# Kernel tuning notes

Measured on AMD Instinct MI355X. Metric: run time of the kernel, lower is better.

Reference implementation:

```python
import jax, jax.numpy as jnp
import numpy as np

N = 50000
E = 800000
BN_EPS = 1e-5


def setup_inputs() -> dict:
    key = jax.random.key(0)
    ks = jax.random.split(key, 8)
    x = jax.random.normal(ks[0], (N, 64), dtype=jnp.float32)
    edge_index = jax.random.randint(ks[1], (2, E), 0, N, dtype=jnp.int64)
    edge_attr = jax.random.uniform(ks[2], (E,), dtype=jnp.float32)
    # GraphConv layer 1: lin_rel (with bias) + lin_root (no bias), 64 -> 128
    W1_rel = jax.random.normal(ks[3], (64, 128), dtype=jnp.float32) / np.sqrt(64)
    b1 = jnp.zeros((128,), dtype=jnp.float32)
    W1_root = jax.random.normal(ks[4], (64, 128), dtype=jnp.float32) / np.sqrt(64)
    # BatchNorm1d(128) affine params
    gamma = jnp.ones((128,), dtype=jnp.float32)
    beta = jnp.zeros((128,), dtype=jnp.float32)
    # GraphConv layer 2: 128 -> 32
    W2_rel = jax.random.normal(ks[5], (128, 32), dtype=jnp.float32) / np.sqrt(128)
    b2 = jnp.zeros((32,), dtype=jnp.float32)
    W2_root = jax.random.normal(ks[6], (128, 32), dtype=jnp.float32) / np.sqrt(128)
    return {"x": x, "edge_attr": edge_attr, "W1_rel": W1_rel, "b1": b1,
            "W1_root": W1_root, "gamma": gamma, "beta": beta,
            "W2_rel": W2_rel, "b2": b2, "W2_root": W2_root,
            "edge_index": edge_index}


def graph_conv(x, edge_index, edge_weight, W_rel, b_rel, W_root):
    # PyG GraphConv (aggr='add'): out = lin_rel(scatter_add(w_e * x[src] -> dst)) + lin_root(x)
    src, dst = edge_index[0], edge_index[1]
    msg = x[src] * edge_weight[:, None]              # [E, F] gather + scale
    agg = jax.ops.segment_sum(msg, dst, num_segments=x.shape[0])  # [N, F]
    return agg @ W_rel + b_rel + x @ W_root


def batch_norm_train(h, gamma, beta):
    mean = jnp.mean(h, axis=0)
    var = jnp.var(h, axis=0)  # biased, as torch uses for normalization
    return (h - mean) * jax.lax.rsqrt(var + BN_EPS) * gamma + beta


def reference(x, edge_attr, W1_rel, b1, W1_root, gamma, beta, W2_rel, b2, W2_root, edge_index):
    h = graph_conv(x, edge_index, edge_attr, W1_rel, b1, W1_root)
    h = batch_norm_train(h, gamma, beta)
    h = jnp.tanh(h)
    out = graph_conv(h, edge_index, edge_attr, W2_rel, b2, W2_root)
    return out
```

## Files before the change

kernel.cpp:

```cpp
#include <hip/hip_runtime.h>
#include <hip/hip_bf16.h>


#define NB 256
#define CAPB 4096
#define LCAP 16
#define CHUNK 2048
#define CAP 32
#define MAXROWS 196
#define OVF_CAP 131072

typedef __bf16 bf16x8 __attribute__((ext_vector_type(8)));
typedef float f32x4 __attribute__((ext_vector_type(4)));

__device__ __forceinline__ void atomAdd(float* p, float v) { unsafeAtomicAdd(p, v); }

__device__ __forceinline__ unsigned packrec(unsigned src, float w) {
    __bf16 bw = (__bf16)w;
    unsigned short us = *(unsigned short*)&bw;
    return (src << 16) | (unsigned)us;
}

__global__ __launch_bounds__(256) void init_k(
    const float* __restrict__ W1rel, const float* __restrict__ W1root,
    const float* __restrict__ W2rel, const float* __restrict__ W2root,
    __bf16* __restrict__ W1t, __bf16* __restrict__ W2t,
    int* __restrict__ gcnt, int* __restrict__ ovfcnt,
    float* __restrict__ bnsum, float* __restrict__ bnsq) {
    if (blockIdx.x == 0) {
        int t = threadIdx.x;
        if (t < NB) gcnt[t] = 0;
        if (t == 0) *ovfcnt = 0;
        if (t < 128) { bnsum[t] = 0.f; bnsq[t] = 0.f; }
    }
    int idx = blockIdx.x * 256 + threadIdx.x;
    if (idx < 128 * 128) {
        int n = idx >> 7, k = idx & 127;
        float v = (k < 64) ? W1rel[k * 128 + n] : W1root[(k - 64) * 128 + n];
        W1t[n * 128 + k] = (__bf16)v;
    } else if (idx < 128 * 128 + 64 * 128) {
        int j = idx - 128 * 128;
        int n = j >> 7, k = j & 127;
        float v = (n < 32) ? W2rel[k * 32 + n] : W2root[k * 32 + (n - 32)];
        W2t[n * 128 + k] = (__bf16)v;
    }
}

__global__ __launch_bounds__(256) void partx_k(
    const float* __restrict__ x, __bf16* __restrict__ xb, int xcB,
    const float* __restrict__ ea, const void* __restrict__ ei,
    int* __restrict__ gcnt, uint2* __restrict__ part,
    int* __restrict__ ovfcnt, int4* __restrict__ ovf, int E, int N) {
    __shared__ int s_flag;
    __shared__ int hist[NB];
    __shared__ int gb[NB];
    __shared__ uint2 stage[NB * LCAP];

    if ((int)blockIdx.x < xcB) {
        int j = blockIdx.x * 256 + threadIdx.x;
        if (j < N * 8) {
            const float4* xs = (const float4*)(x + (size_t)j * 8);
            float4 a = xs[0], b = xs[1];
            bf16x8 v;
            v[0] = (__bf16)a.x; v[1] = (__bf16)a.y; v[2] = (__bf16)a.z; v[3] = (__bf16)a.w;
            v[4] = (__bf16)b.x; v[5] = (__bf16)b.y; v[6] = (__bf16)b.z; v[7] = (__bf16)b.w;
            *(bf16x8*)(xb + (size_t)j * 8) = v;
        }
        return;
    }
    const int pb = blockIdx.x - xcB;

    if (threadIdx.x < 64) {
        const long long* p = (const long long*)ei;
        long long v = p[threadIdx.x & 15];
        int ok = (v >= 0 && v < (long long)N);
        unsigned long long m = __ballot(ok);
        if (threadIdx.x == 0) s_flag = (~m == 0ull) ? 1 : 0;
    }
    for (int i = threadIdx.x; i < NB; i += 256) hist[i] = 0;
    __syncthreads();
    const bool is64 = (s_flag != 0);

    const int base = pb * CHUNK + threadIdx.x * 8;
    int n = E - base; n = n < 0 ? 0 : (n > 8 ? 8 : n);

    int srcs[8], dsts[8]; float wv[8];
    if (n > 0) {
        if (is64) {
            const long long* p = (const long long*)ei;
            if (n == 8 && ((E & 1) == 0)) {
#pragma unroll
                for (int k = 0; k < 4; k++) {
                    int4 a = *(const int4*)(p + base + 2 * k);
                    srcs[2 * k] = a.x; srcs[2 * k + 1] = a.z;
                }
#pragma unroll
                for (int k = 0; k < 4; k++) {
                    int4 b = *(const int4*)(p + E + base + 2 * k);
                    dsts[2 * k] = b.x; dsts[2 * k + 1] = b.z;
                }
            } else {
                for (int k = 0; k < n; k++) { srcs[k] = (int)p[base + k]; dsts[k] = (int)p[E + base + k]; }
            }
        } else {
            const int* p = (const int*)ei;
            if (n == 8 && ((E & 3) == 0)) {
                int4 a0 = *(const int4*)(p + base);
                int4 a1 = *(const int4*)(p + base + 4);
                srcs[0] = a0.x; srcs[1] = a0.y; srcs[2] = a0.z; srcs[3] = a0.w;
                srcs[4] = a1.x; srcs[5] = a1.y; srcs[6] = a1.z; srcs[7] = a1.w;
                int4 b0 = *(const int4*)(p + E + base);
                int4 b1 = *(const int4*)(p + E + base + 4);
                dsts[0] = b0.x; dsts[1] = b0.y; dsts[2] = b0.z; dsts[3] = b0.w;
                dsts[4] = b1.x; dsts[5] = b1.y; dsts[6] = b1.z; dsts[7] = b1.w;
            } else {
                for (int k = 0; k < n; k++) { srcs[k] = p[base + k]; dsts[k] = p[E + base + k]; }
            }
        }
        if (n == 8) {
            float4 w0 = *(const float4*)(ea + base);
            float4 w1 = *(const float4*)(ea + base + 4);
            wv[0] = w0.x; wv[1] = w0.y; wv[2] = w0.z; wv[3] = w0.w;
            wv[4] = w1.x; wv[5] = w1.y; wv[6] = w1.z; wv[7] = w1.w;
        } else {
            for (int k = 0; k < n; k++) wv[k] = ea[base + k];
        }

        int bk[8], pos[8], loc[8];
#pragma unroll
        for (int k = 0; k < 8; k++) {
            if (k < n) {
                unsigned b = ((unsigned)dsts[k] << 8) / (unsigned)N;
                int r0 = (int)((b * (unsigned)N + 255u) >> 8);
                bk[k] = (int)b;
                loc[k] = dsts[k] - r0;
                pos[k] = atomicAdd(&hist[b], 1);
            }
        }
#pragma unroll
        for (int k = 0; k < 8; k++) {
            if (k < n) {
                unsigned packed = ((unsigned)loc[k] << 24) | (unsigned)srcs[k];
                if (pos[k] < LCAP) {
                    stage[bk[k] * LCAP + pos[k]] = make_uint2(packed, __float_as_uint(wv[k]));
                } else {
                    int g = atomicAdd(&gcnt[bk[k]], 1);
                    if (g < CAPB) {
                        part[(size_t)bk[k] * CAPB + g] = make_uint2(packed, __float_as_uint(wv[k]));
                    } else {
                        int o = atomicAdd(ovfcnt, 1);
                        if (o < OVF_CAP) ovf[o] = make_int4(srcs[k], dsts[k], (int)__float_as_uint(wv[k]), 0);
                    }
                }
            }
        }
    }
    __syncthreads();
    if (threadIdx.x < NB) {
        int h = hist[threadIdx.x]; if (h > LCAP) h = LCAP;
        hist[threadIdx.x] = h;
        gb[threadIdx.x] = h ? atomicAdd(&gcnt[threadIdx.x], h) : 0;
    }
    __syncthreads();
    const int wvi = threadIdx.x >> 6;
    const int sub = (threadIdx.x >> 4) & 3;
    const int f = threadIdx.x & 15;
    for (int round = 0; round < 16; ++round) {
        int b = wvi * 64 + round * 4 + sub;
        int h = hist[b];
        if (f < h) {
            int g = gb[b] + f;
            uint2 r = stage[b * LCAP + f];
            if (g < CAPB) {
                part[(size_t)b * CAPB + g] = r;
            } else {
                int r0 = (b * N + 255) >> 8;
                int dst = r0 + (int)(r.x >> 24);
                int o = atomicAdd(ovfcnt, 1);
                if (o < OVF_CAP) ovf[o] = make_int4((int)(r.x & 0xFFFFFFu), dst, (int)r.y, 0);
            }
        }
    }
}

__global__ __launch_bounds__(256) void binscat_k(
    const int* __restrict__ gcnt, const uint2* __restrict__ part,
    unsigned* __restrict__ bins, int* __restrict__ cnt,
    int* __restrict__ ovfcnt, int4* __restrict__ ovf, int N) {
    __shared__ unsigned stage[MAXROWS * CAP];
    __shared__ int lcnt[MAXROWS];
    const int b = blockIdx.x;
    const int r0 = (b * N + 255) >> 8;
    int r1 = ((b + 1) * N + 255) >> 8; if (r1 > N) r1 = N;
    const int rows = r1 - r0;
    for (int i = threadIdx.x; i < rows; i += 256) lcnt[i] = 0;
    __syncthreads();

    int m = gcnt[b]; if (m > CAPB) m = CAPB;
    const uint2* pb = part + (size_t)b * CAPB;
    for (int i = threadIdx.x; i < m; i += 256) {
        uint2 r = pb[i];
        int d = r.x >> 24;
        unsigned src = r.x & 0xFFFFFFu;
        float w = __uint_as_float(r.y);
        int pos = atomicAdd(&lcnt[d], 1);
        if (pos < CAP) {
            stage[d * CAP + pos] = packrec(src, w);
        } else {
            int o = atomicAdd(ovfcnt, 1);
            if (o < OVF_CAP) ovf[o] = make_int4((int)src, r0 + d, (int)r.y, 0);
        }
    }
    __syncthreads();
    uint4* dst = (uint4*)(bins + (size_t)r0 * CAP);
    const uint4* srcp = (const uint4*)stage;
    for (int i = threadIdx.x; i < rows * (CAP / 4); i += 256) dst[i] = srcp[i];
    for (int i = threadIdx.x; i < rows; i += 256) cnt[r0 + i] = lcnt[i];
}

__global__ __launch_bounds__(256) void spmm1_k(
    const __bf16* __restrict__ xb, const int* __restrict__ cntg,
    const unsigned* __restrict__ bins, const int* __restrict__ ovfcnt,
    const int4* __restrict__ ovf, __bf16* __restrict__ aggb, int N) {
    const int lane = threadIdx.x & 63;
    const int sub = lane >> 5;
    const int fp = lane & 31;
    const int row = (blockIdx.x * 256 + threadIdx.x) >> 6;
    if (row >= N) return;
    int cf = cntg[row];
    int cnt = cf > CAP ? CAP : cf;
    unsigned eg = 0u;
    if (lane < cnt) eg = bins[(size_t)row * CAP + lane];
    float ax = 0.f, ay = 0.f;
    for (int j = 0; j < cnt; j += 8) {
        int ss[4]; float ww[4]; unsigned uv[4];
#pragma unroll
        for (int k = 0; k < 4; k++) {
            int idx = j + 2 * k + sub;
            bool ok = idx < cnt;
            unsigned r = (unsigned)__shfl((int)eg, idx);
            ss[k] = ok ? (int)(r >> 16) : 0;
            ww[k] = ok ? __uint_as_float((r & 0xFFFFu) << 16) : 0.f;
        }
#pragma unroll
        for (int k = 0; k < 4; k++)
            uv[k] = *(const unsigned*)((const char*)xb + (size_t)ss[k] * 128 + fp * 4);
#pragma unroll
        for (int k = 0; k < 4; k++) {
            ax = fmaf(ww[k], __uint_as_float((uv[k] & 0xFFFFu) << 16), ax);
            ay = fmaf(ww[k], __uint_as_float(uv[k] & 0xFFFF0000u), ay);
        }
    }
    if (cf > CAP && sub == 0) {
        int nv = *ovfcnt; if (nv > OVF_CAP) nv = OVF_CAP;
        for (int i = 0; i < nv; i++) {
            int4 t = ovf[i];
            if (t.y == row) {
                float w = __uint_as_float((unsigned)t.z);
                unsigned u = *(const unsigned*)((const char*)xb + (size_t)t.x * 128 + fp * 4);
                ax = fmaf(w, __uint_as_float((u & 0xFFFFu) << 16), ax);
                ay = fmaf(w, __uint_as_float(u & 0xFFFF0000u), ay);
            }
        }
    }
    ax += __shfl_xor(ax, 32);
    ay += __shfl_xor(ay, 32);
    if (sub == 0) {
        __bf16 b0 = (__bf16)ax, b1 = (__bf16)ay;
        unsigned pack = (unsigned)*(unsigned short*)&b0 |
                        ((unsigned)*(unsigned short*)&b1 << 16);
        *(unsigned*)((char*)aggb + (size_t)row * 128 + fp * 4) = pack;
    }
}

__global__ __launch_bounds__(256) void gemm1_k(
    const __bf16* __restrict__ aggb, const __bf16* __restrict__ xb,
    const __bf16* __restrict__ W1t, const float* __restrict__ b1,
    __bf16* __restrict__ hb, float* __restrict__ bnsum, float* __restrict__ bnsq,
    int N) {
    __shared__ char Wl[128 * 256];
    __shared__ float redS[4][128];
    __shared__ float redQ[4][128];
    const int t = threadIdx.x;
    for (int i = t; i < 2048; i += 256) {
        int byte = i * 16;
        int row = byte >> 8;
        int sw = byte ^ ((row & 7) << 4);
        *(uint4*)(Wl + sw) = *(const uint4*)((const char*)W1t + byte);
    }

    const int lane = t & 63;
    const int w = t >> 6;
    const int rrow = lane & 15;
    const int q = lane >> 4;
    const int rowbase = blockIdx.x * 128 + w * 32;
    const int ar0 = rowbase + rrow;
    const int ar1 = rowbase + 16 + rrow;
    const int ar0c = (ar0 < N) ? ar0 : (N - 1);
    const int ar1c = (ar1 < N) ? ar1 : (N - 1);

    f32x4 acc0[8], acc1[8];
#pragma unroll
    for (int cb = 0; cb < 8; cb++) {
        acc0[cb][0] = 0.f; acc0[cb][1] = 0.f; acc0[cb][2] = 0.f; acc0[cb][3] = 0.f;
        acc1[cb][0] = 0.f; acc1[cb][1] = 0.f; acc1[cb][2] = 0.f; acc1[cb][3] = 0.f;
    }
    __syncthreads();

#pragma unroll
    for (int ks = 0; ks < 4; ks++) {
        const int koff = (ks & 1) * 32 + q * 8;
        const __bf16* base = (ks < 2) ? aggb : xb;
        bf16x8 a0 = *(const bf16x8*)(base + (size_t)ar0c * 64 + koff);
        bf16x8 a1 = *(const bf16x8*)(base + (size_t)ar1c * 64 + koff);
#pragma unroll
        for (int cb = 0; cb < 8; cb++) {
            int byte = (cb * 16 + rrow) * 256 + ks * 64 + q * 16;
            byte ^= ((rrow & 7) << 4);
            bf16x8 b = *(const bf16x8*)(Wl + byte);
            acc0[cb] = __builtin_amdgcn_mfma_f32_16x16x32_bf16(a0, b, acc0[cb], 0, 0, 0);
            acc1[cb] = __builtin_amdgcn_mfma_f32_16x16x32_bf16(a1, b, acc1[cb], 0, 0, 0);
        }
    }

    float s[8], qs[8];
#pragma unroll
    for (int cb = 0; cb < 8; cb++) {
        const int col = cb * 16 + rrow;
        const float bc = b1[col];
        float ls = 0.f, lq = 0.f;
#pragma unroll
        for (int r = 0; r < 4; r++) {
            int rr0 = rowbase + 4 * q + r;
            if (rr0 < N) {
                float v = acc0[cb][r] + bc;
                hb[(size_t)rr0 * 128 + col] = (__bf16)v;
                ls += v; lq += v * v;
            }
            int rr1 = rowbase + 16 + 4 * q + r;
            if (rr1 < N) {
                float v = acc1[cb][r] + bc;
                hb[(size_t)rr1 * 128 + col] = (__bf16)v;
                ls += v; lq += v * v;
            }
        }
        s[cb] = ls; qs[cb] = lq;
    }
#pragma unroll
    for (int cb = 0; cb < 8; cb++) {
        s[cb] += __shfl_xor(s[cb], 16);  s[cb] += __shfl_xor(s[cb], 32);
        qs[cb] += __shfl_xor(qs[cb], 16); qs[cb] += __shfl_xor(qs[cb], 32);
    }
    if (q == 0) {
#pragma unroll
        for (int cb = 0; cb < 8; cb++) {
            redS[w][cb * 16 + rrow] = s[cb];
            redQ[w][cb * 16 + rrow] = qs[cb];
        }
    }
    __syncthreads();
    if (t < 128) {
        atomAdd(&bnsum[t], redS[0][t] + redS[1][t] + redS[2][t] + redS[3][t]);
    } else {
        int c = t - 128;
        atomAdd(&bnsq[c], redQ[0][c] + redQ[1][c] + redQ[2][c] + redQ[3][c]);
    }
}

__global__ __launch_bounds__(256) void gemm2_k(
    const __bf16* __restrict__ hb, const float* __restrict__ bnsum,
    const float* __restrict__ bnsq, const float* __restrict__ gamma,
    const float* __restrict__ beta, const __bf16* __restrict__ W2t,
    const float* __restrict__ b2, __bf16* __restrict__ y2b,
    float* __restrict__ out, int N) {
    __shared__ char Wl[64 * 256];
    __shared__ float scs[128], shs[128];
    const int t = threadIdx.x;
    for (int i = t; i < 1024; i += 256) {
        int byte = i * 16;
        int row = byte >> 8;
        int sw = byte ^ ((row & 7) << 4);
        *(uint4*)(Wl + sw) = *(const uint4*)((const char*)W2t + byte);
    }
    if (t < 128) {
        float inv = 1.0f / (float)N;
        float mean = bnsum[t] * inv;
        float var = bnsq[t] * inv - mean * mean;
        if (var < 0.f) var = 0.f;
        float sc = gamma[t] * rsqrtf(var + 1e-5f);
        scs[t] = sc;
        shs[t] = beta[t] - mean * sc;
    }

    const int lane = t & 63;
    const int w = t >> 6;
    const int rrow = lane & 15;
    const int q = lane >> 4;
    const int rowbase = blockIdx.x * 128 + w * 32;
    const int ar0 = rowbase + rrow;
    const int ar1 = rowbase + 16 + rrow;
    const int ar0c = (ar0 < N) ? ar0 : (N - 1);
    const int ar1c = (ar1 < N) ? ar1 : (N - 1);

    f32x4 acc0[4], acc1[4];
#pragma unroll
    for (int cb = 0; cb < 4; cb++) {
        acc0[cb][0] = 0.f; acc0[cb][1] = 0.f; acc0[cb][2] = 0.f; acc0[cb][3] = 0.f;
        acc1[cb][0] = 0.f; acc1[cb][1] = 0.f; acc1[cb][2] = 0.f; acc1[cb][3] = 0.f;
    }
    __syncthreads();

#pragma unroll
    for (int ks = 0; ks < 4; ks++) {
        const int k0 = ks * 32 + q * 8;
        bf16x8 hv0 = *(const bf16x8*)(hb + (size_t)ar0c * 128 + k0);
        bf16x8 hv1 = *(const bf16x8*)(hb + (size_t)ar1c * 128 + k0);
        bf16x8 a0, a1;
#pragma unroll
        for (int i = 0; i < 8; i++) {
            float sc = scs[k0 + i], sh = shs[k0 + i];
            a0[i] = (__bf16)tanhf(fmaf((float)hv0[i], sc, sh));
            a1[i] = (__bf16)tanhf(fmaf((float)hv1[i], sc, sh));
        }
#pragma unroll
        for (int cb = 0; cb < 4; cb++) {
            int byte = (cb * 16 + rrow) * 256 + ks * 64 + q * 16;
            byte ^= ((rrow & 7) << 4);
            bf16x8 b = *(const bf16x8*)(Wl + byte);
            acc0[cb] = __builtin_amdgcn_mfma_f32_16x16x32_bf16(a0, b, acc0[cb], 0, 0, 0);
            acc1[cb] = __builtin_amdgcn_mfma_f32_16x16x32_bf16(a1, b, acc1[cb], 0, 0, 0);
        }
    }

#pragma unroll
    for (int cb = 0; cb < 4; cb++) {
        const int col = cb * 16 + rrow;
        const bool isRel = (col < 32);
        const int cc = isRel ? col : (col - 32);
        const float bc = isRel ? 0.f : b2[cc];
#pragma unroll
        for (int r = 0; r < 4; r++) {
            int rr0 = rowbase + 4 * q + r;
            if (rr0 < N) {
                if (isRel) y2b[(size_t)rr0 * 32 + cc] = (__bf16)acc0[cb][r];
                else       out[(size_t)rr0 * 32 + cc] = acc0[cb][r] + bc;
            }
            int rr1 = rowbase + 16 + 4 * q + r;
            if (rr1 < N) {
                if (isRel) y2b[(size_t)rr1 * 32 + cc] = (__bf16)acc1[cb][r];
                else       out[(size_t)rr1 * 32 + cc] = acc1[cb][r] + bc;
            }
        }
    }
}

__global__ __launch_bounds__(256) void spmm2_k(
    const __bf16* __restrict__ y2b, const int* __restrict__ cntg,
    const unsigned* __restrict__ bins, const int* __restrict__ ovfcnt,
    const int4* __restrict__ ovf, float* __restrict__ out, int N) {
    const int lane = threadIdx.x & 63;
    const int qs = lane >> 4;
    const int fp = lane & 15;
    const int row = (blockIdx.x * 256 + threadIdx.x) >> 6;
    if (row >= N) return;
    int cf = cntg[row];
    int cnt = cf > CAP ? CAP : cf;
    unsigned eg = 0u;
    if (lane < cnt) eg = bins[(size_t)row * CAP + lane];
    float ax = 0.f, ay = 0.f;
    for (int j = 0; j < cnt; j += 8) {
        int ss[2]; float ww[2]; unsigned uv[2];
#pragma unroll
        for (int k = 0; k < 2; k++) {
            int idx = j + 4 * k + qs;
            bool ok = idx < cnt;
            unsigned r = (unsigned)__shfl((int)eg, idx);
            ss[k] = ok ? (int)(r >> 16) : 0;
            ww[k] = ok ? __uint_as_float((r & 0xFFFFu) << 16) : 0.f;
        }
#pragma unroll
        for (int k = 0; k < 2; k++)
            uv[k] = *(const unsigned*)((const char*)y2b + (size_t)ss[k] * 64 + fp * 4);
#pragma unroll
        for (int k = 0; k < 2; k++) {
            ax = fmaf(ww[k], __uint_as_float((uv[k] & 0xFFFFu) << 16), ax);
            ay = fmaf(ww[k], __uint_as_float(uv[k] & 0xFFFF0000u), ay);
        }
    }
    if (cf > CAP && qs == 0) {
        int nv = *ovfcnt; if (nv > OVF_CAP) nv = OVF_CAP;
        for (int i = 0; i < nv; i++) {
            int4 t = ovf[i];
            if (t.y == row) {
                float w = __uint_as_float((unsigned)t.z);
                unsigned u = *(const unsigned*)((const char*)y2b + (size_t)t.x * 64 + fp * 4);
                ax = fmaf(w, __uint_as_float((u & 0xFFFFu) << 16), ax);
                ay = fmaf(w, __uint_as_float(u & 0xFFFF0000u), ay);
            }
        }
    }
    ax += __shfl_xor(ax, 16); ax += __shfl_xor(ax, 32);
    ay += __shfl_xor(ay, 16); ay += __shfl_xor(ay, 32);
    if (qs == 0) {
        float2* p = (float2*)((char*)out + (size_t)row * 128 + fp * 8);
        float2 c = *p;
        c.x += ax; c.y += ay;
        *p = c;
    }
}

extern "C" void kernel_launch(void* const* d_in, const int* in_sizes, int n_in,
                              void* d_out, int out_size, void* d_ws, size_t ws_size,
                              hipStream_t stream) {
    const float* x      = (const float*)d_in[0];
    const float* ea     = (const float*)d_in[1];
    const float* W1rel  = (const float*)d_in[2];
    const float* b1     = (const float*)d_in[3];
    const float* W1root = (const float*)d_in[4];
    const float* gamma  = (const float*)d_in[5];
    const float* beta   = (const float*)d_in[6];
    const float* W2rel  = (const float*)d_in[7];
    const float* b2     = (const float*)d_in[8];
    const float* W2root = (const float*)d_in[9];
    const void*  ei     = d_in[10];

    const int N = in_sizes[0] / 64;
    const int E = in_sizes[1];
    const int nbg = (N + 127) / 128;

    char* ws = (char*)d_ws;
    size_t off = 0;
    int*      gcnt    = (int*)     (ws + off); off += NB * 4;
    int*      ovfcnt  = (int*)     (ws + off); off += 256;
    float*    bnsum   = (float*)   (ws + off); off += 512;
    float*    bnsq    = (float*)   (ws + off); off += 512;
    int*      cnt     = (int*)     (ws + off); off += ((size_t)N * 4 + 255) & ~255ull;
    __bf16*   xb      = (__bf16*)  (ws + off); off += (size_t)N * 64 * 2;
    __bf16*   aggb    = (__bf16*)  (ws + off); off += (size_t)N * 64 * 2;
    __bf16*   hb      = (__bf16*)  (ws + off); off += (size_t)N * 128 * 2;
    __bf16*   y2b     = (__bf16*)  (ws + off); off += (size_t)N * 32 * 2;
    uint2*    part    = (uint2*)   (ws + off); off += (size_t)NB * CAPB * 8;
    unsigned* bins    = (unsigned*)(ws + off); off += (size_t)N * CAP * 4;
    int4*     ovf     = (int4*)    (ws + off); off += (size_t)OVF_CAP * 16;
    __bf16*   W1t     = (__bf16*)  (ws + off); off += 128 * 128 * 2;
    __bf16*   W2t     = (__bf16*)  (ws + off); off += 64 * 128 * 2;

    init_k<<<96, 256, 0, stream>>>(W1rel, W1root, W2rel, W2root, W1t, W2t,
                                   gcnt, ovfcnt, bnsum, bnsq);
    const int xcB = (N * 8 + 255) / 256;
    const int partB = (E + CHUNK - 1) / CHUNK;
    partx_k<<<xcB + partB, 256, 0, stream>>>(x, xb, xcB, ea, ei, gcnt, part,
                                             ovfcnt, ovf, E, N);
    binscat_k<<<NB, 256, 0, stream>>>(gcnt, part, bins, cnt, ovfcnt, ovf, N);
    const int rowBlocks = (N * 64 + 255) / 256;
    spmm1_k<<<rowBlocks, 256, 0, stream>>>(xb, cnt, bins, ovfcnt, ovf, aggb, N);
    gemm1_k<<<nbg, 256, 0, stream>>>(aggb, xb, W1t, b1, hb, bnsum, bnsq, N);
    gemm2_k<<<nbg, 256, 0, stream>>>(hb, bnsum, bnsq, gamma, beta, W2t, b2, y2b,
                                     (float*)d_out, N);
    spmm2_k<<<rowBlocks, 256, 0, stream>>>(y2b, cnt, bins, ovfcnt, ovf, (float*)d_out, N);
}
```

Before: 112.7 us.

## Recompute layer-1 GEMM in gemm2 instead of storing hidden activations

gemm1 now only accumulates BatchNorm statistics and no longer writes the N x 128 bf16 hidden tensor. gemm2 recomputes the layer-1 GEMM from aggb and xb, stages the result in shared memory, then applies BN and tanh before the layer-2 MFMA. This trades a 12.8 MB global write and read for duplicated layer-1 MFMA work and a larger shared-memory footprint in gemm2 (about 50 KB), which may lower occupancy.

```diff
diff --git a/kernel.cpp b/kernel.cpp
--- a/kernel.cpp
+++ b/kernel.cpp
@@ -276,8 +276,7 @@
 __global__ __launch_bounds__(256) void gemm1_k(
     const __bf16* __restrict__ aggb, const __bf16* __restrict__ xb,
     const __bf16* __restrict__ W1t, const float* __restrict__ b1,
-    __bf16* __restrict__ hb, float* __restrict__ bnsum, float* __restrict__ bnsq,
-    int N) {
+    float* __restrict__ bnsum, float* __restrict__ bnsq, int N) {
     __shared__ char Wl[128 * 256];
     __shared__ float redS[4][128];
     __shared__ float redQ[4][128];
@@ -334,13 +333,11 @@
             int rr0 = rowbase + 4 * q + r;
             if (rr0 < N) {
                 float v = acc0[cb][r] + bc;
-                hb[(size_t)rr0 * 128 + col] = (__bf16)v;
                 ls += v; lq += v * v;
             }
             int rr1 = rowbase + 16 + 4 * q + r;
             if (rr1 < N) {
                 float v = acc1[cb][r] + bc;
-                hb[(size_t)rr1 * 128 + col] = (__bf16)v;
                 ls += v; lq += v * v;
             }
         }
@@ -368,19 +365,27 @@
 }
 
 __global__ __launch_bounds__(256) void gemm2_k(
-    const __bf16* __restrict__ hb, const float* __restrict__ bnsum,
-    const float* __restrict__ bnsq, const float* __restrict__ gamma,
-    const float* __restrict__ beta, const __bf16* __restrict__ W2t,
-    const float* __restrict__ b2, __bf16* __restrict__ y2b,
-    float* __restrict__ out, int N) {
-    __shared__ char Wl[64 * 256];
-    __shared__ float scs[128], shs[128];
+    const __bf16* __restrict__ aggb, const __bf16* __restrict__ xb,
+    const __bf16* __restrict__ W1t, const float* __restrict__ b1,
+    const float* __restrict__ bnsum, const float* __restrict__ bnsq,
+    const float* __restrict__ gamma, const float* __restrict__ beta,
+    const __bf16* __restrict__ W2t, const float* __restrict__ b2,
+    __bf16* __restrict__ y2b, float* __restrict__ out, int N) {
+    __shared__ char Wl[128 * 256];
+    __shared__ char W2l[64 * 256];
+    __shared__ float scs[128], shs[128], b1s[128];
     const int t = threadIdx.x;
+    for (int i = t; i < 2048; i += 256) {
+        int byte = i * 16;
+        int row = byte >> 8;
+        int sw = byte ^ ((row & 7) << 4);
+        *(uint4*)(Wl + sw) = *(const uint4*)((const char*)W1t + byte);
+    }
     for (int i = t; i < 1024; i += 256) {
         int byte = i * 16;
         int row = byte >> 8;
         int sw = byte ^ ((row & 7) << 4);
-        *(uint4*)(Wl + sw) = *(const uint4*)((const char*)W2t + byte);
+        *(uint4*)(W2l + sw) = *(const uint4*)((const char*)W2t + byte);
     }
     if (t < 128) {
         float inv = 1.0f / (float)N;
@@ -390,6 +395,7 @@
         float sc = gamma[t] * rsqrtf(var + 1e-5f);
         scs[t] = sc;
         shs[t] = beta[t] - mean * sc;
+        b1s[t] = b1[t];
     }
 
     const int lane = t & 63;
@@ -402,9 +408,9 @@
     const int ar0c = (ar0 < N) ? ar0 : (N - 1);
     const int ar1c = (ar1 < N) ? ar1 : (N - 1);
 
-    f32x4 acc0[4], acc1[4];
-#pragma unroll
-    for (int cb = 0; cb < 4; cb++) {
+    f32x4 acc0[8], acc1[8];
+#pragma unroll
+    for (int cb = 0; cb < 8; cb++) {
         acc0[cb][0] = 0.f; acc0[cb][1] = 0.f; acc0[cb][2] = 0.f; acc0[cb][3] = 0.f;
         acc1[cb][0] = 0.f; acc1[cb][1] = 0.f; acc1[cb][2] = 0.f; acc1[cb][3] = 0.f;
     }
@@ -412,18 +418,12 @@
 
 #pragma unroll
     for (int ks = 0; ks < 4; ks++) {
-        const int k0 = ks * 32 + q * 8;
-        bf16x8 hv0 = *(const bf16x8*)(hb + (size_t)ar0c * 128 + k0);
-        bf16x8 hv1 = *(const bf16x8*)(hb + (size_t)ar1c * 128 + k0);
-        bf16x8 a0, a1;
-#pragma unroll
-        for (int i = 0; i < 8; i++) {
-            float sc = scs[k0 + i], sh = shs[k0 + i];
-            a0[i] = (__bf16)tanhf(fmaf((float)hv0[i], sc, sh));
-            a1[i] = (__bf16)tanhf(fmaf((float)hv1[i], sc, sh));
-        }
-#pragma unroll
-        for (int cb = 0; cb < 4; cb++) {
+        const int koff = (ks & 1) * 32 + q * 8;
+        const __bf16* base = (ks < 2) ? aggb : xb;
+        bf16x8 a0 = *(const bf16x8*)(base + (size_t)ar0c * 64 + koff);
+        bf16x8 a1 = *(const bf16x8*)(base + (size_t)ar1c * 64 + koff);
+#pragma unroll
+        for (int cb = 0; cb < 8; cb++) {
             int byte = (cb * 16 + rrow) * 256 + ks * 64 + q * 16;
             byte ^= ((rrow & 7) << 4);
             bf16x8 b = *(const bf16x8*)(Wl + byte);
@@ -431,6 +431,56 @@
             acc1[cb] = __builtin_amdgcn_mfma_f32_16x16x32_bf16(a1, b, acc1[cb], 0, 0, 0);
         }
     }
+    __syncthreads();
+
+#pragma unroll
+    for (int cb = 0; cb < 8; cb++) {
+        const int col = cb * 16 + rrow;
+        const float bc = b1s[col];
+#pragma unroll
+        for (int r = 0; r < 4; r++) {
+            int lrow0 = w * 32 + 4 * q + r;
+            int byte0 = (lrow0 * 256 + col * 2) ^ ((lrow0 & 7) << 4);
+            *(__bf16*)(Wl + byte0) = (__bf16)(acc0[cb][r] + bc);
+            int lrow1 = lrow0 + 16;
+            int byte1 = (lrow1 * 256 + col * 2) ^ ((lrow1 & 7) << 4);
+            *(__bf16*)(Wl + byte1) = (__bf16)(acc1[cb][r] + bc);
+        }
+    }
+    __syncthreads();
+
+    f32x4 bcc0[4], bcc1[4];
+#pragma unroll
+    for (int cb = 0; cb < 4; cb++) {
+        bcc0[cb][0] = 0.f; bcc0[cb][1] = 0.f; bcc0[cb][2] = 0.f; bcc0[cb][3] = 0.f;
+        bcc1[cb][0] = 0.f; bcc1[cb][1] = 0.f; bcc1[cb][2] = 0.f; bcc1[cb][3] = 0.f;
+    }
+    const int lrowA0 = w * 32 + rrow;
+    const int lrowA1 = lrowA0 + 16;
+
+#pragma unroll
+    for (int ks = 0; ks < 4; ks++) {
+        const int k0 = ks * 32 + q * 8;
+        int byteA0 = (lrowA0 * 256 + k0 * 2) ^ ((lrowA0 & 7) << 4);
+        int byteA1 = (lrowA1 * 256 + k0 * 2) ^ ((lrowA1 & 7) << 4);
+        bf16x8 hv0 = *(const bf16x8*)(Wl + byteA0);
+        bf16x8 hv1 = *(const bf16x8*)(Wl + byteA1);
+        bf16x8 a0, a1;
+#pragma unroll
+        for (int i = 0; i < 8; i++) {
+            float sc = scs[k0 + i], sh = shs[k0 + i];
+            a0[i] = (__bf16)tanhf(fmaf((float)hv0[i], sc, sh));
+            a1[i] = (__bf16)tanhf(fmaf((float)hv1[i], sc, sh));
+        }
+#pragma unroll
+        for (int cb = 0; cb < 4; cb++) {
+            int byte = (cb * 16 + rrow) * 256 + ks * 64 + q * 16;
+            byte ^= ((rrow & 7) << 4);
+            bf16x8 b = *(const bf16x8*)(W2l + byte);
+            bcc0[cb] = __builtin_amdgcn_mfma_f32_16x16x32_bf16(a0, b, bcc0[cb], 0, 0, 0);
+            bcc1[cb] = __builtin_amdgcn_mfma_f32_16x16x32_bf16(a1, b, bcc1[cb], 0, 0, 0);
+        }
+    }
 
 #pragma unroll
     for (int cb = 0; cb < 4; cb++) {
@@ -442,13 +492,13 @@
         for (int r = 0; r < 4; r++) {
             int rr0 = rowbase + 4 * q + r;
             if (rr0 < N) {
-                if (isRel) y2b[(size_t)rr0 * 32 + cc] = (__bf16)acc0[cb][r];
-                else       out[(size_t)rr0 * 32 + cc] = acc0[cb][r] + bc;
+                if (isRel) y2b[(size_t)rr0 * 32 + cc] = (__bf16)bcc0[cb][r];
+                else       out[(size_t)rr0 * 32 + cc] = bcc0[cb][r] + bc;
             }
             int rr1 = rowbase + 16 + 4 * q + r;
             if (rr1 < N) {
-                if (isRel) y2b[(size_t)rr1 * 32 + cc] = (__bf16)acc1[cb][r];
-                else       out[(size_t)rr1 * 32 + cc] = acc1[cb][r] + bc;
+                if (isRel) y2b[(size_t)rr1 * 32 + cc] = (__bf16)bcc1[cb][r];
+                else       out[(size_t)rr1 * 32 + cc] = bcc1[cb][r] + bc;
             }
         }
     }
@@ -537,7 +587,6 @@
     int*      cnt     = (int*)     (ws + off); off += ((size_t)N * 4 + 255) & ~255ull;
     __bf16*   xb      = (__bf16*)  (ws + off); off += (size_t)N * 64 * 2;
     __bf16*   aggb    = (__bf16*)  (ws + off); off += (size_t)N * 64 * 2;
-    __bf16*   hb      = (__bf16*)  (ws + off); off += (size_t)N * 128 * 2;
     __bf16*   y2b     = (__bf16*)  (ws + off); off += (size_t)N * 32 * 2;
     uint2*    part    = (uint2*)   (ws + off); off += (size_t)NB * CAPB * 8;
     unsigned* bins    = (unsigned*)(ws + off); off += (size_t)N * CAP * 4;
@@ -554,8 +603,8 @@
     binscat_k<<<NB, 256, 0, stream>>>(gcnt, part, bins, cnt, ovfcnt, ovf, N);
     const int rowBlocks = (N * 64 + 255) / 256;
     spmm1_k<<<rowBlocks, 256, 0, stream>>>(xb, cnt, bins, ovfcnt, ovf, aggb, N);
-    gemm1_k<<<nbg, 256, 0, stream>>>(aggb, xb, W1t, b1, hb, bnsum, bnsq, N);
-    gemm2_k<<<nbg, 256, 0, stream>>>(hb, bnsum, bnsq, gamma, beta, W2t, b2, y2b,
-                                     (float*)d_out, N);
+    gemm1_k<<<nbg, 256, 0, stream>>>(aggb, xb, W1t, b1, bnsum, bnsq, N);
+    gemm2_k<<<nbg, 256, 0, stream>>>(aggb, xb, W1t, b1, bnsum, bnsq, gamma, beta,
+                                     W2t, b2, y2b, (float*)d_out, N);
     spmm2_k<<<rowBlocks, 256, 0, stream>>>(y2b, cnt, bins, ovfcnt, ovf, (float*)d_out, N);
 }
```

After: 108.0 us (median of 2 runs). 4.2% less time.
